# Kernel tuning notes

Measured on AMD Instinct MI355X. Metric: run time of the kernel, lower is better.

The kernel has to match this reference:

```python
import jax, jax.numpy as jnp
import numpy as np

N = 30000
F_IN = 500
HID = 16
OUT = 3
E = 960000


def setup_inputs() -> dict:
    key = jax.random.key(0)
    ks = jax.random.split(key, 10)
    x = jax.random.normal(ks[0], (N, F_IN), dtype=jnp.float32)
    edge_index = jax.random.randint(ks[1], (2, E), 0, N, dtype=jnp.int32)
    # CNN params (torch Conv1d: weight [out, in, k], bias [out])
    s1 = 1.0 / np.sqrt(1 * 3)
    s2 = 1.0 / np.sqrt(HID * 3)
    conv1_w = jax.random.uniform(ks[2], (HID, 1, 3), jnp.float32, -s1, s1)
    conv1_b = jax.random.uniform(ks[3], (HID,), jnp.float32, -s1, s1)
    conv2_w = jax.random.uniform(ks[4], (HID, HID, 3), jnp.float32, -s2, s2)
    conv2_b = jax.random.uniform(ks[5], (HID,), jnp.float32, -s2, s2)
    # GCNConv params (glorot weight [in, out], zero bias)
    g1 = np.sqrt(6.0 / (HID + HID))
    g2 = np.sqrt(6.0 / (HID + OUT))
    gcn1_w = jax.random.uniform(ks[6], (HID, HID), jnp.float32, -g1, g1)
    gcn1_b = jnp.zeros((HID,), jnp.float32)
    gcn2_w = jax.random.uniform(ks[7], (HID, OUT), jnp.float32, -g2, g2)
    gcn2_b = jnp.zeros((OUT,), jnp.float32)
    return {"x": x, "conv1_w": conv1_w, "conv1_b": conv1_b,
            "conv2_w": conv2_w, "conv2_b": conv2_b,
            "gcn1_w": gcn1_w, "gcn1_b": gcn1_b,
            "gcn2_w": gcn2_w, "gcn2_b": gcn2_b,
            "edge_index": edge_index}


def _conv1d(x, w, b):
    # x: [N, C_in, L], w: [C_out, C_in, 3], padding=1
    y = jax.lax.conv_general_dilated(
        x, w, window_strides=(1,), padding=[(1, 1)],
        dimension_numbers=("NCH", "OIH", "NCH"))
    return y + b[None, :, None]


def _gcn_conv(x, w, b, src, dst, n):
    # x: [n, d_in] -> [n, d_out]; Kipf normalization with self-loops
    h = x @ w
    loop = jnp.arange(n, dtype=src.dtype)
    s = jnp.concatenate([src, loop])
    d = jnp.concatenate([dst, loop])
    deg = jax.ops.segment_sum(jnp.ones_like(d, dtype=h.dtype), d, num_segments=n)
    dinv = jnp.where(deg > 0, jax.lax.rsqrt(deg), 0.0)
    norm = dinv[s] * dinv[d]                      # [E+n]
    msg = h[s] * norm[:, None]                    # gather + scale
    return jax.ops.segment_sum(msg, d, num_segments=n) + b


def reference(x, conv1_w, conv1_b, conv2_w, conv2_b,
              gcn1_w, gcn1_b, gcn2_w, gcn2_b, edge_index):
    # CNN feature extractor over feature axis
    h = x[:, None, :]                             # [N, 1, F_IN]
    h = jax.nn.relu(_conv1d(h, conv1_w, conv1_b))  # [N, HID, F_IN]
    h = jax.nn.relu(_conv1d(h, conv2_w, conv2_b))  # [N, HID, F_IN]
    h = jnp.max(h, axis=2)                        # global max pool -> [N, HID]
    # GCN
    src, dst = edge_index[0], edge_index[1]
    n = h.shape[0]
    h = jax.nn.relu(_gcn_conv(h, gcn1_w, gcn1_b, src, dst, n))
    h = _gcn_conv(h, gcn2_w, gcn2_b, src, dst, n)  # [N, OUT]
    return jax.nn.log_softmax(h, axis=1)
```

## Files before the change

kernel.cpp:

```cpp
#include <hip/hip_runtime.h>
#include <hip/hip_bf16.h>

#define N_NODES 30000
#define F_INLEN 500
#define HID 16
#define OUTC 3
#define NEDGE 960000
#define YPITCH 20
#define NBIN 938
#define HBLK 128
#define EPRH (NEDGE / HBLK)
#define ECAP 1536

typedef float  f32x4 __attribute__((ext_vector_type(4)));
typedef float  f32x2 __attribute__((ext_vector_type(2)));
typedef short  s16x8 __attribute__((ext_vector_type(8)));

static __device__ __forceinline__ unsigned short f2bf(float f) {
    unsigned int u = __float_as_uint(f);
    unsigned int r = (u + 0x7fffu + ((u >> 16) & 1u)) >> 16;
    return (unsigned short)r;
}
static __device__ __forceinline__ unsigned int pack_bf16x2(float v0, float v1) {
#if __has_builtin(__builtin_amdgcn_cvt_pk_bf16_f32)
    typedef __bf16 bf16x2_t __attribute__((ext_vector_type(2)));
    union { bf16x2_t v; unsigned int u; } cv;
    cv.v = __builtin_amdgcn_cvt_pk_bf16_f32(v0, v1);
    return cv.u;
#else
    return __builtin_amdgcn_perm(__float_as_uint(v1), __float_as_uint(v0), 0x07060302);
#endif
}

__global__ __launch_bounds__(256) void hist_kernel(
    const float* __restrict__ w2, short* __restrict__ bfragsG,
    const int* __restrict__ dst, int* __restrict__ degi, int* __restrict__ cntbase)
{
    const int tid = threadIdx.x;
    if (blockIdx.x == HBLK) {
        if (tid < 64) {
            const int n16 = tid & 15, q = tid >> 4;
#pragma unroll
            for (int j = 0; j < 8; j++) {
                {
                    const int c = q * 8 + j;
                    const int t = c >> 4, i = c & 15;
                    bfragsG[tid * 16 + j] = (short)f2bf(w2[n16 * 48 + i * 3 + t]);
                }
                {
                    const int c = 32 + q * 8 + j;
                    short v = 0;
                    if (c < 48) { const int t = c >> 4, i = c & 15; v = (short)f2bf(w2[n16 * 48 + i * 3 + t]); }
                    bfragsG[tid * 16 + 8 + j] = v;
                }
            }
        }
        return;
    }
    __shared__ int histH[NBIN];
    for (int i = tid; i < NBIN; i += 256) histH[i] = 0;
    __syncthreads();
    const int e0 = blockIdx.x * EPRH;
    for (int e = e0 + tid; e < e0 + EPRH; e += 256) {
        const int d = dst[e];
        atomicAdd(&histH[d >> 5], 1);
        atomicAdd(&degi[d], 1);
    }
    __syncthreads();
    for (int i = tid; i < NBIN; i += 256) cntbase[blockIdx.x * NBIN + i] = histH[i];
}

__global__ __launch_bounds__(256, 7) void conv_reorder(
    const float* __restrict__ x,
    const float* __restrict__ w1, const float* __restrict__ b1,
    const float* __restrict__ b2, const short* __restrict__ bfragsG,
    const int* __restrict__ src, const int* __restrict__ dst,
    const int* __restrict__ degi, const int* __restrict__ cntbase,
    int* __restrict__ packed, int* __restrict__ binstart,
    float* __restrict__ h0)
{
    __shared__ __align__(16) float xp[502];
    __shared__ __align__(16) unsigned short yh[516 * YPITCH];
    __shared__ float red[64];

    const int tid = threadIdx.x;

    if (blockIdx.x < HBLK) {
        int* scA    = (int*)yh;
        int* scB    = scA + NBIN;
        int* totb   = scB + NBIN;
        int* cursor = totb + NBIN;
        const int blk = blockIdx.x;
        for (int bin = tid; bin < NBIN; bin += 256) {
            int tot = 0, psum = 0;
            for (int k = 0; k < HBLK; k++) {
                const int c = cntbase[k * NBIN + bin];
                tot += c;
                if (k < blk) psum += c;
            }
            scA[bin]    = tot;
            totb[bin]   = tot;
            cursor[bin] = psum;
        }
        __syncthreads();
        int* pA = scA; int* pB = scB;
        for (int off = 1; off < NBIN; off <<= 1) {
            for (int i = tid; i < NBIN; i += 256)
                pB[i] = pA[i] + ((i >= off) ? pA[i - off] : 0);
            __syncthreads();
            int* tp = pA; pA = pB; pB = tp;
        }
        for (int i = tid; i < NBIN; i += 256) {
            const int excl = pA[i] - totb[i];
            cursor[i] += excl;
            if (blk == 0) binstart[i] = excl;
        }
        if (blk == 0 && tid == 0) binstart[NBIN] = NEDGE;
        __syncthreads();
        const int e0 = blk * EPRH;
        for (int e = e0 + tid; e < e0 + EPRH; e += 256) {
            const int d = dst[e];
            const int pos = atomicAdd(&cursor[d >> 5], 1);
            packed[pos] = src[e] | (d << 15);
        }
        return;
    }

    const int node = blockIdx.x - HBLK;
    const int lane = tid & 63;
    const int wave = tid >> 6;
    const int n16  = lane & 15;
    const int q    = lane >> 4;

    if (tid == 0) { xp[0] = 0.f; xp[501] = 0.f; }
    if (tid < 125) {
        const float4 v = ((const float4*)(x + (long long)node * F_INLEN))[tid];
        xp[4 * tid + 1] = v.x; xp[4 * tid + 2] = v.y;
        xp[4 * tid + 3] = v.z; xp[4 * tid + 4] = v.w;
    }
    {
        const int ri = tid >> 4;
        const int row = (ri == 0) ? 0 : (500 + ri);
        yh[row * YPITCH + (tid & 15)] = 0;
    }
    const s16x8* bfp = (const s16x8*)(bfragsG + lane * 16);
    const s16x8 bh0 = bfp[0], bh1 = bfp[1];

    f32x2 wt0[8], wt1[8], wt2[8], bb[8];
#pragma unroll
    for (int cp = 0; cp < 8; cp++) {
        const int c0 = 2 * cp, c1 = 2 * cp + 1;
        wt0[cp] = (f32x2){w1[c0 * 3 + 0], w1[c1 * 3 + 0]};
        wt1[cp] = (f32x2){w1[c0 * 3 + 1], w1[c1 * 3 + 1]};
        wt2[cp] = (f32x2){w1[c0 * 3 + 2], w1[c1 * 3 + 2]};
        bb[cp]  = (f32x2){b1[c0], b1[c1]};
    }
    __syncthreads();

    for (int p = tid; p < 500; p += 256) {
        const float x0 = xp[p], x1 = xp[p + 1], x2 = xp[p + 2];
        const f32x2 xv0 = {x0, x0}, xv1 = {x1, x1}, xv2 = {x2, x2};
        const f32x2 zero = {0.f, 0.f};
        unsigned int hp[8];
#pragma unroll
        for (int cp = 0; cp < 8; cp++) {
            f32x2 a = bb[cp];
            a = __builtin_elementwise_fma(wt0[cp], xv0, a);
            a = __builtin_elementwise_fma(wt1[cp], xv1, a);
            a = __builtin_elementwise_fma(wt2[cp], xv2, a);
            a = __builtin_elementwise_max(a, zero);
            hp[cp] = pack_bf16x2(a[0], a[1]);
        }
        uint2* d = (uint2*)&yh[(p + 1) * YPITCH];
        d[0] = make_uint2(hp[0], hp[1]);
        d[1] = make_uint2(hp[2], hp[3]);
        d[2] = make_uint2(hp[4], hp[5]);
        d[3] = make_uint2(hp[6], hp[7]);
    }
    __syncthreads();

    struct S8 { short4 lo, hi; };
    float mx0 = -3.0e38f, mx1 = -3.0e38f, mx2 = -3.0e38f, mx3 = -3.0e38f;
#pragma unroll
    for (int it = 0; it < 8; it++) {
        const int tile = wave * 8 + it;
        const int p0 = tile * 16 + n16;
        const int cA = (q & 1) * 8;
        const int rA = p0 + (q >> 1);
        const int rB = p0 + 2 + (q >> 1);
        S8 t0, t1;
        t0.lo = *(const short4*)&yh[rA * YPITCH + cA];
        t0.hi = *(const short4*)&yh[rA * YPITCH + cA + 4];
        t1.lo = *(const short4*)&yh[rB * YPITCH + cA];
        t1.hi = *(const short4*)&yh[rB * YPITCH + cA + 4];
        const s16x8 ah0 = *(const s16x8*)&t0;
        const s16x8 ah1 = *(const s16x8*)&t1;
        f32x4 acc = {0.f, 0.f, 0.f, 0.f};
        acc = __builtin_amdgcn_mfma_f32_16x16x32_bf16(ah0, bh0, acc, 0, 0, 0);
        acc = __builtin_amdgcn_mfma_f32_16x16x32_bf16(ah1, bh1, acc, 0, 0, 0);
        if (it < 7) {
            mx0 = fmaxf(mx0, acc[0]);
            mx1 = fmaxf(mx1, acc[1]);
            mx2 = fmaxf(mx2, acc[2]);
            mx3 = fmaxf(mx3, acc[3]);
        } else if (wave < 3) {
            mx0 = fmaxf(mx0, acc[0]);
            mx1 = fmaxf(mx1, acc[1]);
            mx2 = fmaxf(mx2, acc[2]);
            mx3 = fmaxf(mx3, acc[3]);
        } else if (q == 0) {
            mx0 = fmaxf(mx0, acc[0]);
            mx1 = fmaxf(mx1, acc[1]);
            mx2 = fmaxf(mx2, acc[2]);
            mx3 = fmaxf(mx3, acc[3]);
        }
    }
    float m = fmaxf(fmaxf(mx0, mx1), fmaxf(mx2, mx3));
    m = fmaxf(m, __shfl_xor(m, 16));
    m = fmaxf(m, __shfl_xor(m, 32));
    if (lane < 16) red[wave * 16 + lane] = m;
    __syncthreads();
    if (tid < 16) {
        const float mm = fmaxf(fmaxf(red[tid], red[16 + tid]), fmaxf(red[32 + tid], red[48 + tid]));
        const float dv = rsqrtf((float)(degi[node] + 1));
        h0[node * HID + tid] = fmaxf(mm + b2[tid], 0.f) * dv;
    }
}

__global__ __launch_bounds__(256) void agg1_kernel(
    const int* __restrict__ binstart, int* __restrict__ packed,
    const float* __restrict__ h0,
    const float* __restrict__ W1, const float* __restrict__ b1g,
    const float* __restrict__ W2, float4* __restrict__ t2p4,
    int* __restrict__ binofs)
{
    __shared__ float w1s[256];
    __shared__ float w2s[48];
    __shared__ float b1s[16];
    __shared__ float accS[32 * 17];
    __shared__ int eL[ECAP];
    __shared__ int srt[ECAP];
    __shared__ int h32[32], ls32[32], lofs32[32];
    const int tid = threadIdx.x;
    const int blk = blockIdx.x;
    w1s[tid] = W1[tid];
    if (tid < 48) w2s[tid] = W2[tid];
    if (tid < 16) b1s[tid] = b1g[tid];
    if (tid < 32) h32[tid] = 0;
    const int beg = binstart[blk];
    const int cnt = binstart[blk + 1] - beg;
    __syncthreads();
    for (int j = tid; j < cnt; j += 256) {
        const int p = packed[beg + j];
        eL[j] = p;
        atomicAdd(&h32[(p >> 15) & 31], 1);
    }
    __syncthreads();
    if (tid < 32) {
        const int v = h32[tid];
        int inc = v;
#pragma unroll
        for (int off = 1; off < 32; off <<= 1) {
            const int y = __shfl_up(inc, off);
            if (tid >= off) inc += y;
        }
        ls32[tid] = inc - v;
        lofs32[tid] = inc - v;
    }
    __syncthreads();
    for (int j = tid; j < cnt; j += 256) {
        const int p = eL[j];
        const int pos = atomicAdd(&lofs32[(p >> 15) & 31], 1);
        srt[pos] = p;
    }
    __syncthreads();
    for (int j = tid; j < cnt; j += 256) packed[beg + j] = srt[j];
    if (tid < 32) {
        binofs[blk * 64 + tid]      = ls32[tid];
        binofs[blk * 64 + 32 + tid] = h32[tid];
    }
    const int n = tid >> 3;
    const int eslot = (tid >> 2) & 1;
    const int q = tid & 3;
    const int node = blk * 32 + n;
    const bool valid = node < N_NODES;
    f32x4 acc = {0.f, 0.f, 0.f, 0.f};
    if (valid) {
        const int s0 = ls32[n];
        const int s1 = s0 + h32[n];
        for (int i = s0 + eslot; i < s1; i += 2) {
            const int s = srt[i] & 32767;
            acc += *(const f32x4*)(h0 + s * HID + q * 4);
        }
    }
#pragma unroll
    for (int c = 0; c < 4; c++) acc[c] += __shfl_xor(acc[c], 4);
    if (valid && eslot == 0) {
        acc += *(const f32x4*)(h0 + node * HID + q * 4);
        accS[n * 17 + q * 4 + 0] = acc[0];
        accS[n * 17 + q * 4 + 1] = acc[1];
        accS[n * 17 + q * 4 + 2] = acc[2];
        accS[n * 17 + q * 4 + 3] = acc[3];
    }
    __syncthreads();
    if (tid < 128) {
        const int n2 = tid >> 2;
        const int node2 = blk * 32 + n2;
        if (node2 < N_NODES) {
            const float dv = rsqrtf((float)(h32[n2] + 1));
            const int q2 = tid & 3;
            float y0 = 0.f, y1 = 0.f, y2 = 0.f, y3 = 0.f;
#pragma unroll
            for (int i = 0; i < 16; i++) {
                const float a = accS[n2 * 17 + i];
                y0 = fmaf(a, w1s[i * 16 + q2 * 4 + 0], y0);
                y1 = fmaf(a, w1s[i * 16 + q2 * 4 + 1], y1);
                y2 = fmaf(a, w1s[i * 16 + q2 * 4 + 2], y2);
                y3 = fmaf(a, w1s[i * 16 + q2 * 4 + 3], y3);
            }
            float d0 = 0.f, d1 = 0.f, d2 = 0.f;
            const float yv[4] = {y0, y1, y2, y3};
#pragma unroll
            for (int j = 0; j < 4; j++) {
                const int o = q2 * 4 + j;
                const float h = fmaxf(b1s[o] + dv * yv[j], 0.f);
                d0 = fmaf(h, w2s[o * 3 + 0], d0);
                d1 = fmaf(h, w2s[o * 3 + 1], d1);
                d2 = fmaf(h, w2s[o * 3 + 2], d2);
            }
            d0 += __shfl_xor(d0, 1); d0 += __shfl_xor(d0, 2);
            d1 += __shfl_xor(d1, 1); d1 += __shfl_xor(d1, 2);
            d2 += __shfl_xor(d2, 1); d2 += __shfl_xor(d2, 2);
            if (q2 == 0) t2p4[node2] = make_float4(d0 * dv, d1 * dv, d2 * dv, dv);
        }
    }
}

__global__ __launch_bounds__(256) void agg2_kernel(
    const int* __restrict__ binstart, const int* __restrict__ packed,
    const float4* __restrict__ t2p4, const int* __restrict__ binofs,
    const float* __restrict__ b2g, float* __restrict__ out)
{
    __shared__ int eL[ECAP];
    __shared__ int ofs[64];
    const int tid = threadIdx.x;
    const int blk = blockIdx.x;
    const int beg = binstart[blk];
    const int cnt = binstart[blk + 1] - beg;
    if (tid < 64) ofs[tid] = binofs[blk * 64 + tid];
    for (int j = tid; j < cnt; j += 256) eL[j] = packed[beg + j];
    __syncthreads();
    const int n = tid >> 3;
    const int ln8 = tid & 7;
    const int node = blk * 32 + n;
    float a0 = 0.f, a1 = 0.f, a2 = 0.f;
    if (node < N_NODES) {
        const int s0 = ofs[n];
        const int s1 = s0 + ofs[32 + n];
        for (int i = s0 + ln8; i < s1; i += 8) {
            const int s = eL[i] & 32767;
            const float4 v = t2p4[s];
            a0 += v.x; a1 += v.y; a2 += v.z;
        }
    }
#pragma unroll
    for (int msk = 1; msk < 8; msk <<= 1) {
        a0 += __shfl_xor(a0, msk);
        a1 += __shfl_xor(a1, msk);
        a2 += __shfl_xor(a2, msk);
    }
    if (ln8 == 0 && node < N_NODES) {
        const float4 self = t2p4[node];
        const float dv = self.w;
        const float z0 = b2g[0] + dv * (a0 + self.x);
        const float z1 = b2g[1] + dv * (a1 + self.y);
        const float z2 = b2g[2] + dv * (a2 + self.z);
        const float m = fmaxf(z0, fmaxf(z1, z2));
        const float lg = m + logf(expf(z0 - m) + expf(z1 - m) + expf(z2 - m));
        out[node * 3 + 0] = z0 - lg;
        out[node * 3 + 1] = z1 - lg;
        out[node * 3 + 2] = z2 - lg;
    }
}

extern "C" void kernel_launch(void* const* d_in, const int* in_sizes, int n_in,
                              void* d_out, int out_size, void* d_ws, size_t ws_size,
                              hipStream_t stream)
{
    const float* x   = (const float*)d_in[0];
    const float* w1  = (const float*)d_in[1];
    const float* b1  = (const float*)d_in[2];
    const float* w2  = (const float*)d_in[3];
    const float* b2  = (const float*)d_in[4];
    const float* g1w = (const float*)d_in[5];
    const float* g1b = (const float*)d_in[6];
    const float* g2w = (const float*)d_in[7];
    const float* g2b = (const float*)d_in[8];
    const int*   ei  = (const int*)d_in[9];
    const int* src = ei;
    const int* dst = ei + NEDGE;

    float* ws = (float*)d_ws;
    float*  h0      = ws;
    float4* t2p4    = (float4*)(ws + 480000);
    int*    degi    = (int*)(ws + 600000);
    int*    cntbase = (int*)(ws + 630000);
    int*    binstart= (int*)(ws + 750064);
    int*    packed  = (int*)(ws + 751104);
    int*    binofs  = (int*)(ws + 1711104);
    short*  bfragsG = (short*)(ws + 1771136);
    float*  out     = (float*)d_out;

    hipMemsetAsync(degi, 0, N_NODES * sizeof(int), stream);
    hist_kernel<<<HBLK + 1, 256, 0, stream>>>(w2, bfragsG, dst, degi, cntbase);
    conv_reorder<<<HBLK + N_NODES, 256, 0, stream>>>(x, w1, b1, b2, bfragsG,
                                                     src, dst, degi, cntbase,
                                                     packed, binstart, h0);
    agg1_kernel<<<NBIN, 256, 0, stream>>>(binstart, packed, h0,
                                          g1w, g1b, g2w, t2p4, binofs);
    agg2_kernel<<<NBIN, 256, 0, stream>>>(binstart, packed, t2p4, binofs, g2b, out);
}
```

Before: 223.4 us.

## Fuse both GCN aggregation kernels into one persistent kernel with grid barrier

```diff
diff --git a/kernel.cpp b/kernel.cpp
--- a/kernel.cpp
+++ b/kernel.cpp
@@ -11,6 +11,8 @@
 #define HBLK 128
 #define EPRH (NEDGE / HBLK)
 #define ECAP 1536
+#define ABLK 256
+#define BPB 4
 
 typedef float  f32x4 __attribute__((ext_vector_type(4)));
 typedef float  f32x2 __attribute__((ext_vector_type(2)));
@@ -227,12 +229,13 @@
     }
 }
 
-__global__ __launch_bounds__(256) void agg1_kernel(
+__global__ __launch_bounds__(1024) void agg_fused(
     const int* __restrict__ binstart, int* __restrict__ packed,
     const float* __restrict__ h0,
     const float* __restrict__ W1, const float* __restrict__ b1g,
-    const float* __restrict__ W2, float4* __restrict__ t2p4,
-    int* __restrict__ binofs)
+    const float* __restrict__ W2, const float* __restrict__ b2g,
+    float4* __restrict__ t2p4, int* __restrict__ binofs,
+    float* __restrict__ out, int* __restrict__ bar)
 {
     __shared__ float w1s[256];
     __shared__ float w2s[48];
@@ -243,143 +246,158 @@
     __shared__ int h32[32], ls32[32], lofs32[32];
     const int tid = threadIdx.x;
     const int blk = blockIdx.x;
-    w1s[tid] = W1[tid];
-    if (tid < 48) w2s[tid] = W2[tid];
-    if (tid < 16) b1s[tid] = b1g[tid];
-    if (tid < 32) h32[tid] = 0;
-    const int beg = binstart[blk];
-    const int cnt = binstart[blk + 1] - beg;
-    __syncthreads();
-    for (int j = tid; j < cnt; j += 256) {
-        const int p = packed[beg + j];
-        eL[j] = p;
-        atomicAdd(&h32[(p >> 15) & 31], 1);
-    }
-    __syncthreads();
-    if (tid < 32) {
-        const int v = h32[tid];
-        int inc = v;
-#pragma unroll
-        for (int off = 1; off < 32; off <<= 1) {
-            const int y = __shfl_up(inc, off);
-            if (tid >= off) inc += y;
-        }
-        ls32[tid] = inc - v;
-        lofs32[tid] = inc - v;
-    }
-    __syncthreads();
-    for (int j = tid; j < cnt; j += 256) {
-        const int p = eL[j];
-        const int pos = atomicAdd(&lofs32[(p >> 15) & 31], 1);
-        srt[pos] = p;
-    }
-    __syncthreads();
-    for (int j = tid; j < cnt; j += 256) packed[beg + j] = srt[j];
-    if (tid < 32) {
-        binofs[blk * 64 + tid]      = ls32[tid];
-        binofs[blk * 64 + 32 + tid] = h32[tid];
-    }
-    const int n = tid >> 3;
-    const int eslot = (tid >> 2) & 1;
-    const int q = tid & 3;
-    const int node = blk * 32 + n;
-    const bool valid = node < N_NODES;
-    f32x4 acc = {0.f, 0.f, 0.f, 0.f};
-    if (valid) {
-        const int s0 = ls32[n];
-        const int s1 = s0 + h32[n];
-        for (int i = s0 + eslot; i < s1; i += 2) {
-            const int s = srt[i] & 32767;
-            acc += *(const f32x4*)(h0 + s * HID + q * 4);
-        }
-    }
-#pragma unroll
-    for (int c = 0; c < 4; c++) acc[c] += __shfl_xor(acc[c], 4);
-    if (valid && eslot == 0) {
-        acc += *(const f32x4*)(h0 + node * HID + q * 4);
-        accS[n * 17 + q * 4 + 0] = acc[0];
-        accS[n * 17 + q * 4 + 1] = acc[1];
-        accS[n * 17 + q * 4 + 2] = acc[2];
-        accS[n * 17 + q * 4 + 3] = acc[3];
-    }
-    __syncthreads();
-    if (tid < 128) {
-        const int n2 = tid >> 2;
-        const int node2 = blk * 32 + n2;
-        if (node2 < N_NODES) {
-            const float dv = rsqrtf((float)(h32[n2] + 1));
-            const int q2 = tid & 3;
-            float y0 = 0.f, y1 = 0.f, y2 = 0.f, y3 = 0.f;
-#pragma unroll
-            for (int i = 0; i < 16; i++) {
-                const float a = accS[n2 * 17 + i];
-                y0 = fmaf(a, w1s[i * 16 + q2 * 4 + 0], y0);
-                y1 = fmaf(a, w1s[i * 16 + q2 * 4 + 1], y1);
-                y2 = fmaf(a, w1s[i * 16 + q2 * 4 + 2], y2);
-                y3 = fmaf(a, w1s[i * 16 + q2 * 4 + 3], y3);
-            }
-            float d0 = 0.f, d1 = 0.f, d2 = 0.f;
-            const float yv[4] = {y0, y1, y2, y3};
-#pragma unroll
-            for (int j = 0; j < 4; j++) {
-                const int o = q2 * 4 + j;
-                const float h = fmaxf(b1s[o] + dv * yv[j], 0.f);
-                d0 = fmaf(h, w2s[o * 3 + 0], d0);
-                d1 = fmaf(h, w2s[o * 3 + 1], d1);
-                d2 = fmaf(h, w2s[o * 3 + 2], d2);
-            }
-            d0 += __shfl_xor(d0, 1); d0 += __shfl_xor(d0, 2);
-            d1 += __shfl_xor(d1, 1); d1 += __shfl_xor(d1, 2);
-            d2 += __shfl_xor(d2, 1); d2 += __shfl_xor(d2, 2);
-            if (q2 == 0) t2p4[node2] = make_float4(d0 * dv, d1 * dv, d2 * dv, dv);
-        }
-    }
-}
-
-__global__ __launch_bounds__(256) void agg2_kernel(
-    const int* __restrict__ binstart, const int* __restrict__ packed,
-    const float4* __restrict__ t2p4, const int* __restrict__ binofs,
-    const float* __restrict__ b2g, float* __restrict__ out)
-{
-    __shared__ int eL[ECAP];
-    __shared__ int ofs[64];
-    const int tid = threadIdx.x;
-    const int blk = blockIdx.x;
-    const int beg = binstart[blk];
-    const int cnt = binstart[blk + 1] - beg;
-    if (tid < 64) ofs[tid] = binofs[blk * 64 + tid];
-    for (int j = tid; j < cnt; j += 256) eL[j] = packed[beg + j];
-    __syncthreads();
-    const int n = tid >> 3;
-    const int ln8 = tid & 7;
-    const int node = blk * 32 + n;
-    float a0 = 0.f, a1 = 0.f, a2 = 0.f;
-    if (node < N_NODES) {
-        const int s0 = ofs[n];
-        const int s1 = s0 + ofs[32 + n];
-        for (int i = s0 + ln8; i < s1; i += 8) {
-            const int s = eL[i] & 32767;
-            const float4 v = t2p4[s];
-            a0 += v.x; a1 += v.y; a2 += v.z;
-        }
-    }
-#pragma unroll
-    for (int msk = 1; msk < 8; msk <<= 1) {
-        a0 += __shfl_xor(a0, msk);
-        a1 += __shfl_xor(a1, msk);
-        a2 += __shfl_xor(a2, msk);
-    }
-    if (ln8 == 0 && node < N_NODES) {
-        const float4 self = t2p4[node];
-        const float dv = self.w;
-        const float z0 = b2g[0] + dv * (a0 + self.x);
-        const float z1 = b2g[1] + dv * (a1 + self.y);
-        const float z2 = b2g[2] + dv * (a2 + self.z);
-        const float m = fmaxf(z0, fmaxf(z1, z2));
-        const float lg = m + logf(expf(z0 - m) + expf(z1 - m) + expf(z2 - m));
-        out[node * 3 + 0] = z0 - lg;
-        out[node * 3 + 1] = z1 - lg;
-        out[node * 3 + 2] = z2 - lg;
+    if (tid < 256) w1s[tid] = W1[tid];
+    if (tid >= 256 && tid < 304) w2s[tid - 256] = W2[tid - 256];
+    if (tid >= 320 && tid < 336) b1s[tid - 320] = b1g[tid - 320];
+
+    for (int bi = 0; bi < BPB; bi++) {
+        const int bin = blk * BPB + bi;
+        if (bin >= NBIN) break;
+        __syncthreads();
+        if (tid < 32) h32[tid] = 0;
+        const int beg = binstart[bin];
+        const int cnt = binstart[bin + 1] - beg;
+        __syncthreads();
+        for (int j = tid; j < cnt; j += 1024) {
+            const int p = packed[beg + j];
+            eL[j] = p;
+            atomicAdd(&h32[(p >> 15) & 31], 1);
+        }
+        __syncthreads();
+        if (tid < 32) {
+            const int v = h32[tid];
+            int inc = v;
+#pragma unroll
+            for (int off = 1; off < 32; off <<= 1) {
+                const int y = __shfl_up(inc, off);
+                if (tid >= off) inc += y;
+            }
+            ls32[tid] = inc - v;
+            lofs32[tid] = inc - v;
+        }
+        __syncthreads();
+        for (int j = tid; j < cnt; j += 1024) {
+            const int p = eL[j];
+            const int pos = atomicAdd(&lofs32[(p >> 15) & 31], 1);
+            srt[pos] = p;
+        }
+        __syncthreads();
+        for (int j = tid; j < cnt; j += 1024) packed[beg + j] = srt[j];
+        if (tid < 32) {
+            binofs[bin * 64 + tid]      = ls32[tid];
+            binofs[bin * 64 + 32 + tid] = h32[tid];
+        }
+        const int n = tid >> 5;
+        const int sub = tid & 31;
+        const int eslot = sub >> 2;
+        const int q = sub & 3;
+        const int node = bin * 32 + n;
+        const bool valid = node < N_NODES;
+        f32x4 acc = {0.f, 0.f, 0.f, 0.f};
+        if (valid) {
+            const int s0 = ls32[n];
+            const int s1 = s0 + h32[n];
+            for (int i = s0 + eslot; i < s1; i += 8) {
+                const int s = srt[i] & 32767;
+                acc += *(const f32x4*)(h0 + s * HID + q * 4);
+            }
+        }
+#pragma unroll
+        for (int c = 0; c < 4; c++) {
+            acc[c] += __shfl_xor(acc[c], 4);
+            acc[c] += __shfl_xor(acc[c], 8);
+            acc[c] += __shfl_xor(acc[c], 16);
+        }
+        if (valid && eslot == 0) {
+            acc += *(const f32x4*)(h0 + node * HID + q * 4);
+            accS[n * 17 + q * 4 + 0] = acc[0];
+            accS[n * 17 + q * 4 + 1] = acc[1];
+            accS[n * 17 + q * 4 + 2] = acc[2];
+            accS[n * 17 + q * 4 + 3] = acc[3];
+        }
+        __syncthreads();
+        if (tid < 128) {
+            const int n2 = tid >> 2;
+            const int node2 = bin * 32 + n2;
+            if (node2 < N_NODES) {
+                const float dv = rsqrtf((float)(h32[n2] + 1));
+                const int q2 = tid & 3;
+                float y0 = 0.f, y1 = 0.f, y2 = 0.f, y3 = 0.f;
+#pragma unroll
+                for (int i = 0; i < 16; i++) {
+                    const float a = accS[n2 * 17 + i];
+                    y0 = fmaf(a, w1s[i * 16 + q2 * 4 + 0], y0);
+                    y1 = fmaf(a, w1s[i * 16 + q2 * 4 + 1], y1);
+                    y2 = fmaf(a, w1s[i * 16 + q2 * 4 + 2], y2);
+                    y3 = fmaf(a, w1s[i * 16 + q2 * 4 + 3], y3);
+                }
+                float d0 = 0.f, d1 = 0.f, d2 = 0.f;
+                const float yv[4] = {y0, y1, y2, y3};
+#pragma unroll
+                for (int j = 0; j < 4; j++) {
+                    const int o = q2 * 4 + j;
+                    const float h = fmaxf(b1s[o] + dv * yv[j], 0.f);
+                    d0 = fmaf(h, w2s[o * 3 + 0], d0);
+                    d1 = fmaf(h, w2s[o * 3 + 1], d1);
+                    d2 = fmaf(h, w2s[o * 3 + 2], d2);
+                }
+                d0 += __shfl_xor(d0, 1); d0 += __shfl_xor(d0, 2);
+                d1 += __shfl_xor(d1, 1); d1 += __shfl_xor(d1, 2);
+                d2 += __shfl_xor(d2, 1); d2 += __shfl_xor(d2, 2);
+                if (q2 == 0) t2p4[node2] = make_float4(d0 * dv, d1 * dv, d2 * dv, dv);
+            }
+        }
+    }
+
+    __syncthreads();
+    if (tid == 0) {
+        __hip_atomic_fetch_add(bar, 1, __ATOMIC_ACQ_REL, __HIP_MEMORY_SCOPE_AGENT);
+        while (__hip_atomic_load(bar, __ATOMIC_ACQUIRE, __HIP_MEMORY_SCOPE_AGENT) < ABLK)
+            __builtin_amdgcn_s_sleep(64);
+    }
+    __syncthreads();
+
+    for (int bi = 0; bi < BPB; bi++) {
+        const int bin = blk * BPB + bi;
+        if (bin >= NBIN) break;
+        __syncthreads();
+        const int beg = binstart[bin];
+        const int cnt = binstart[bin + 1] - beg;
+        if (tid < 32) ls32[tid] = binofs[bin * 64 + tid];
+        if (tid >= 32 && tid < 64) h32[tid - 32] = binofs[bin * 64 + tid];
+        for (int j = tid; j < cnt; j += 1024) eL[j] = packed[beg + j];
+        __syncthreads();
+        const int n = tid >> 5;
+        const int ln = tid & 31;
+        const int node = bin * 32 + n;
+        float a0 = 0.f, a1 = 0.f, a2 = 0.f;
+        if (node < N_NODES) {
+            const int s0 = ls32[n];
+            const int s1 = s0 + h32[n];
+            for (int i = s0 + ln; i < s1; i += 32) {
+                const int s = eL[i] & 32767;
+                const float4 v = t2p4[s];
+                a0 += v.x; a1 += v.y; a2 += v.z;
+            }
+        }
+#pragma unroll
+        for (int msk = 1; msk < 32; msk <<= 1) {
+            a0 += __shfl_xor(a0, msk);
+            a1 += __shfl_xor(a1, msk);
+            a2 += __shfl_xor(a2, msk);
+        }
+        if (ln == 0 && node < N_NODES) {
+            const float4 self = t2p4[node];
+            const float dv = self.w;
+            const float z0 = b2g[0] + dv * (a0 + self.x);
+            const float z1 = b2g[1] + dv * (a1 + self.y);
+            const float z2 = b2g[2] + dv * (a2 + self.z);
+            const float m = fmaxf(z0, fmaxf(z1, z2));
+            const float lg = m + logf(expf(z0 - m) + expf(z1 - m) + expf(z2 - m));
+            out[node * 3 + 0] = z0 - lg;
+            out[node * 3 + 1] = z1 - lg;
+            out[node * 3 + 2] = z2 - lg;
+        }
     }
 }
 
@@ -404,19 +422,20 @@
     float*  h0      = ws;
     float4* t2p4    = (float4*)(ws + 480000);
     int*    degi    = (int*)(ws + 600000);
-    int*    cntbase = (int*)(ws + 630000);
-    int*    binstart= (int*)(ws + 750064);
+    int*    bar     = (int*)(ws + 630000);
+    int*    cntbase = (int*)(ws + 630016);
+    int*    binstart= (int*)(ws + 750080);
     int*    packed  = (int*)(ws + 751104);
     int*    binofs  = (int*)(ws + 1711104);
     short*  bfragsG = (short*)(ws + 1771136);
     float*  out     = (float*)d_out;
 
-    hipMemsetAsync(degi, 0, N_NODES * sizeof(int), stream);
+    hipMemsetAsync(degi, 0, (N_NODES + 16) * sizeof(int), stream);
     hist_kernel<<<HBLK + 1, 256, 0, stream>>>(w2, bfragsG, dst, degi, cntbase);
     conv_reorder<<<HBLK + N_NODES, 256, 0, stream>>>(x, w1, b1, b2, bfragsG,
                                                      src, dst, degi, cntbase,
                                                      packed, binstart, h0);
-    agg1_kernel<<<NBIN, 256, 0, stream>>>(binstart, packed, h0,
-                                          g1w, g1b, g2w, t2p4, binofs);
-    agg2_kernel<<<NBIN, 256, 0, stream>>>(binstart, packed, t2p4, binofs, g2b, out);
-}
+    agg_fused<<<ABLK, 1024, 0, stream>>>(binstart, packed, h0,
+                                         g1w, g1b, g2w, g2b,
+                                         t2p4, binofs, out, bar);
+}
```

Result: slower. 244.2 us (+9.3%).
